# Kernel optimization log

Measured on AMD Instinct MI355X. Metric: run time of the kernel, lower is better.

## Reference

```python
import jax, jax.numpy as jnp
from jax import lax
import numpy as np

QMAX = 127.0  # int8 symmetric quant range


def setup_inputs() -> dict:
    key = jax.random.key(0)
    k1, k2, k3, k4 = jax.random.split(key, 4)
    B, S, D_in, D_out = 4, 2048, 4096, 4096
    x = jax.random.normal(k1, (B, S, D_in), dtype=jnp.float32)
    # pre-quantized per-channel weights [output_size, input_size]
    weight_q = jax.random.randint(k2, (D_out, D_in), -127, 128, dtype=jnp.int32).astype(jnp.int8)
    weight_scale = (jax.random.uniform(k3, (D_out,), dtype=jnp.float32) + 0.5) * 0.01
    bias = jax.random.normal(k4, (D_out,), dtype=jnp.float32) * 0.02
    return {"x": x, "weight_q": weight_q, "weight_scale": weight_scale, "bias": bias}


def reference(x, weight_q, weight_scale, bias):
    """Dynamic per-token int8 activation quant + int8 matmul + dequant + bias.

    x: [..., D_in] float32; weight_q: [D_out, D_in] int8;
    weight_scale: [D_out]; bias: [D_out]. Returns [..., D_out] float32.
    """
    orig_shape = x.shape
    x2 = x.reshape(-1, orig_shape[-1])  # [T, D_in]
    # dynamic per-token symmetric quantization
    amax = jnp.max(jnp.abs(x2), axis=-1, keepdims=True)  # [T, 1]
    x_scale = jnp.maximum(amax, 1e-8) / QMAX
    x_q = jnp.clip(jnp.round(x2 / x_scale), -128.0, QMAX).astype(jnp.int8)
    acc = lax.dot_general(x_q, weight_q, (((1,), (1,)), ((), ())),
                          preferred_element_type=jnp.int32)  # [T, D_out]
    out = acc.astype(jnp.float32) * x_scale * weight_scale[None, :]
    out = out.reshape(*orig_shape[:-1], out.shape[-1]) + bias
    return out
```

## Files before the change

kernel.cpp:

```cpp
#include <hip/hip_runtime.h>

typedef __attribute__((ext_vector_type(4))) int int4v;

__global__ __launch_bounds__(256) void pack_w_kernel(const int* __restrict__ w32,
                                                     int* __restrict__ w8,
                                                     long n4) {
    long i = (long)blockIdx.x * 256 + threadIdx.x;
    if (i >= n4) return;
    int4v v = ((const int4v*)w32)[i];
    w8[i] = (v[0] & 0xFF) | ((v[1] & 0xFF) << 8) |
            ((v[2] & 0xFF) << 16) | ((v[3] & 0xFF) << 24);
}

template <int NCHUNK>
__global__ __launch_bounds__(256) void quant_kernel(const float* __restrict__ x,
                                                    signed char* __restrict__ xq,
                                                    float* __restrict__ xs,
                                                    int K) {
    const int t = blockIdx.x;
    const int tid = threadIdx.x;
    const float4* row = (const float4*)(x + (size_t)t * K);

    float4 v[NCHUNK];
    float amax = 0.0f;
    #pragma unroll
    for (int i = 0; i < NCHUNK; ++i) {
        float4 f = row[i * 256 + tid];
        v[i] = f;
        amax = fmaxf(amax, fmaxf(fmaxf(fabsf(f.x), fabsf(f.y)),
                                 fmaxf(fabsf(f.z), fabsf(f.w))));
    }
    #pragma unroll
    for (int off = 32; off >= 1; off >>= 1)
        amax = fmaxf(amax, __shfl_xor(amax, off, 64));
    __shared__ float red[4];
    if ((tid & 63) == 0) red[tid >> 6] = amax;
    __syncthreads();
    amax = fmaxf(fmaxf(red[0], red[1]), fmaxf(red[2], red[3]));

    const float scale = fmaxf(amax, 1e-8f) / 127.0f;
    if (tid == 0) xs[t] = scale;
    const float inv = 1.0f / scale;

    int* orow = (int*)(xq + (size_t)t * K);
    #pragma unroll
    for (int i = 0; i < NCHUNK; ++i) {
        float4 f = v[i];
        int q0 = (int)fminf(fmaxf(rintf(f.x * inv), -128.0f), 127.0f);
        int q1 = (int)fminf(fmaxf(rintf(f.y * inv), -128.0f), 127.0f);
        int q2 = (int)fminf(fmaxf(rintf(f.z * inv), -128.0f), 127.0f);
        int q3 = (int)fminf(fmaxf(rintf(f.w * inv), -128.0f), 127.0f);
        orow[i * 256 + tid] =
            (q0 & 0xFF) | ((q1 & 0xFF) << 8) | ((q2 & 0xFF) << 16) | ((q3 & 0xFF) << 24);
    }
}

#define BM 256
#define BN 256
#define BKB 128

#define MFMA_I8 __builtin_amdgcn_mfma_i32_16x16x64_i8

#define BARRIER()                       \
    do {                                \
        __builtin_amdgcn_s_barrier();   \
        asm volatile("" ::: "memory");  \
    } while (0)

#define LGKM0() asm volatile("s_waitcnt lgkmcnt(0)" ::: "memory")
#define VMCNT4() asm volatile("s_waitcnt vmcnt(4)" ::: "memory")

#define STAGE_HALF(GL, LB, ROWOFF, KK)                                        \
    do {                                                                      \
        __builtin_amdgcn_global_load_lds(                                     \
            (const __attribute__((address_space(1))) void*)(                  \
                (GL) + (size_t)(ROWOFF) * K + (KK)),                          \
            (__attribute__((address_space(3))) void*)((LB) + (ROWOFF) * BKB), \
            16, 0, 0);                                                        \
        __builtin_amdgcn_global_load_lds(                                     \
            (const __attribute__((address_space(1))) void*)(                  \
                (GL) + (size_t)((ROWOFF) + 64) * K + (KK)),                   \
            (__attribute__((address_space(3))) void*)(                        \
                (LB) + ((ROWOFF) + 64) * BKB),                                \
            16, 0, 0);                                                        \
    } while (0)

#define LDA_KS(RP, MOFF, SW)                                               \
    do {                                                                   \
        af[0] = *(const int4v*)((RP) + ((MOFF) + 0) * 2048 + (SW));        \
        af[1] = *(const int4v*)((RP) + ((MOFF) + 1) * 2048 + (SW));        \
        af[2] = *(const int4v*)((RP) + ((MOFF) + 2) * 2048 + (SW));        \
        af[3] = *(const int4v*)((RP) + ((MOFF) + 3) * 2048 + (SW));        \
    } while (0)

#define LDB_KS(RP, KS, SW)                                                 \
    do {                                                                   \
        bf[0][(KS)] = *(const int4v*)((RP) + 0 * 2048 + (SW));             \
        bf[1][(KS)] = *(const int4v*)((RP) + 1 * 2048 + (SW));             \
        bf[2][(KS)] = *(const int4v*)((RP) + 2 * 2048 + (SW));             \
        bf[3][(KS)] = *(const int4v*)((RP) + 3 * 2048 + (SW));             \
    } while (0)

#define PH_MFMA(MB, KS)                                                       \
    do {                                                                      \
        _Pragma("unroll") for (int m_ = 0; m_ < 4; ++m_) {                    \
            _Pragma("unroll") for (int n_ = 0; n_ < 4; ++n_) {                \
                acc[(MB) + m_][n_] = MFMA_I8(af[m_], bf[n_][(KS)],            \
                                             acc[(MB) + m_][n_], 0, 0, 0);    \
            }                                                                 \
        }                                                                     \
    } while (0)

__global__ __launch_bounds__(512, 2) void gemm_i8_kernel(
    const signed char* __restrict__ A,
    const signed char* __restrict__ B,
    const float* __restrict__ xs,
    const float* __restrict__ wsc,
    const float* __restrict__ bias,
    float* __restrict__ C,
    int M, int N, int K) {
    __shared__ __align__(16) signed char lds[2][2][BM * BKB];

    const int tid = threadIdx.x;
    const int lane = tid & 63;
    const int wv = tid >> 6;
    const int wrow = wv >> 2;
    const int wcol = wv & 3;
    const int fr = lane & 15;
    const int q = lane >> 4;

    const int bm = blockIdx.y * BM;
    const int bn = blockIdx.x * BN;

    const int srow = wv * 8 + (lane >> 3);
    const int scol = ((lane & 7) ^ ((lane >> 3) & 7)) << 4;
    const signed char* gA = A + (size_t)(bm + srow) * K + scol;
    const signed char* gB = B + (size_t)(bn + srow) * K + scol;

    signed char* wA0 = &lds[0][0][0] + wv * 1024;
    signed char* wA1 = &lds[1][0][0] + wv * 1024;
    signed char* wB0 = &lds[0][1][0] + wv * 1024;
    signed char* wB1 = &lds[1][1][0] + wv * 1024;

    const int rowA = (wrow * 128 + fr) * BKB;
    const int rowB = (wcol * 64 + fr) * BKB;
    const int sw0 = ((0 + q) ^ (fr & 7)) << 4;
    const int sw1 = ((4 + q) ^ (fr & 7)) << 4;
    const signed char* rA0 = &lds[0][0][0] + rowA;
    const signed char* rA1 = &lds[1][0][0] + rowA;
    const signed char* rB0 = &lds[0][1][0] + rowB;
    const signed char* rB1 = &lds[1][1][0] + rowB;

    int4v acc[8][4];
    const int4v zero = {0, 0, 0, 0};
    #pragma unroll
    for (int m = 0; m < 8; ++m)
        #pragma unroll
        for (int n = 0; n < 4; ++n) acc[m][n] = zero;
    int4v af[4];
    int4v bf[4][2];

    STAGE_HALF(gA, wA0, 0, 0);
    STAGE_HALF(gA, wA0, 128, 0);
    STAGE_HALF(gB, wB0, 0, 0);
    STAGE_HALF(gB, wB0, 128, 0);
    STAGE_HALF(gB, wB1, 0, (size_t)BKB);
    STAGE_HALF(gB, wB1, 128, (size_t)BKB);
    VMCNT4();
    BARRIER();

    const int NT = K / BKB;
    for (int i = 0; i < NT / 2; ++i) {
        const size_t kk1 = (size_t)(2 * i + 1) * BKB;
        int t2 = 2 * i + 2; if (t2 >= NT) t2 -= NT;
        int t3 = 2 * i + 3; if (t3 >= NT) t3 -= NT;
        const size_t kk2 = (size_t)t2 * BKB;
        const size_t kk3 = (size_t)t3 * BKB;

        LDA_KS(rA0, 0, sw0);
        LDB_KS(rB0, 0, sw0);
        STAGE_HALF(gA, wA1, 0, kk1);
        BARRIER();
        LGKM0();
        __builtin_amdgcn_s_setprio(1);
        PH_MFMA(0, 0);
        __builtin_amdgcn_s_setprio(0);
        BARRIER();

        LDA_KS(rA0, 0, sw1);
        LDB_KS(rB0, 1, sw1);
        STAGE_HALF(gA, wA1, 128, kk1);
        BARRIER();
        LGKM0();
        __builtin_amdgcn_s_setprio(1);
        PH_MFMA(0, 1);
        __builtin_amdgcn_s_setprio(0);
        BARRIER();

        LDA_KS(rA0, 4, sw0);
        STAGE_HALF(gB, wB0, 0, kk2);
        BARRIER();
        LGKM0();
        __builtin_amdgcn_s_setprio(1);
        PH_MFMA(4, 0);
        __builtin_amdgcn_s_setprio(0);
        BARRIER();

        LDA_KS(rA0, 4, sw1);
        STAGE_HALF(gB, wB0, 128, kk2);
        VMCNT4();
        BARRIER();
        LGKM0();
        __builtin_amdgcn_s_setprio(1);
        PH_MFMA(4, 1);
        __builtin_amdgcn_s_setprio(0);
        BARRIER();

        LDA_KS(rA1, 0, sw0);
        LDB_KS(rB1, 0, sw0);
        STAGE_HALF(gA, wA0, 0, kk2);
        BARRIER();
        LGKM0();
        __builtin_amdgcn_s_setprio(1);
        PH_MFMA(0, 0);
        __builtin_amdgcn_s_setprio(0);
        BARRIER();

        LDA_KS(rA1, 0, sw1);
        LDB_KS(rB1, 1, sw1);
        STAGE_HALF(gA, wA0, 128, kk2);
        BARRIER();
        LGKM0();
        __builtin_amdgcn_s_setprio(1);
        PH_MFMA(0, 1);
        __builtin_amdgcn_s_setprio(0);
        BARRIER();

        LDA_KS(rA1, 4, sw0);
        STAGE_HALF(gB, wB1, 0, kk3);
        BARRIER();
        LGKM0();
        __builtin_amdgcn_s_setprio(1);
        PH_MFMA(4, 0);
        __builtin_amdgcn_s_setprio(0);
        BARRIER();

        LDA_KS(rA1, 4, sw1);
        STAGE_HALF(gB, wB1, 128, kk3);
        VMCNT4();
        BARRIER();
        LGKM0();
        __builtin_amdgcn_s_setprio(1);
        PH_MFMA(4, 1);
        __builtin_amdgcn_s_setprio(0);
        BARRIER();
    }

    asm volatile("s_waitcnt vmcnt(0)" ::: "memory");

    const int cb = bn + wcol * 64;
    float wv4[4], bv4[4];
    #pragma unroll
    for (int n = 0; n < 4; ++n) {
        wv4[n] = wsc[cb + n * 16 + fr];
        bv4[n] = bias[cb + n * 16 + fr];
    }
    #pragma unroll
    for (int m = 0; m < 8; ++m) {
        #pragma unroll
        for (int r = 0; r < 4; ++r) {
            const int row = bm + wrow * 128 + m * 16 + q * 4 + r;
            const float s = xs[row];
            float* crow = C + (size_t)row * N + cb + fr;
            #pragma unroll
            for (int n = 0; n < 4; ++n)
                crow[n * 16] = (float)acc[m][n][r] * s * wv4[n] + bv4[n];
        }
    }
}

extern "C" void kernel_launch(void* const* d_in, const int* in_sizes, int n_in,
                              void* d_out, int out_size, void* d_ws, size_t ws_size,
                              hipStream_t stream) {
    const float* x = (const float*)d_in[0];
    const int* wq32 = (const int*)d_in[1];
    const float* wscale = (const float*)d_in[2];
    const float* bias = (const float*)d_in[3];
    float* out = (float*)d_out;

    const int d_out_dim = in_sizes[2];
    const int d_in_dim = in_sizes[1] / d_out_dim;
    const int T = in_sizes[0] / d_in_dim;

    const size_t wbytes = (size_t)d_out_dim * d_in_dim;
    signed char* w8 = (signed char*)d_ws;
    signed char* xq = (signed char*)d_ws + wbytes;
    float* xscl = (float*)((char*)d_ws + wbytes + (size_t)T * d_in_dim);

    const long n4 = (long)d_out_dim * d_in_dim / 4;
    pack_w_kernel<<<(int)((n4 + 255) / 256), 256, 0, stream>>>(wq32, (int*)w8, n4);

    if (d_in_dim == 4096) {
        quant_kernel<4><<<T, 256, 0, stream>>>(x, xq, xscl, d_in_dim);
    } else {
        quant_kernel<8><<<T, 256, 0, stream>>>(x, xq, xscl, d_in_dim);
    }

    dim3 grid(d_out_dim / BN, T / BM);
    gemm_i8_kernel<<<grid, 512, 0, stream>>>(xq, w8, xscl, wscale, bias, out,
                                             T, d_out_dim, d_in_dim);
}
```

Before: 379.8 us.

## Double-buffer MFMA A/B fragments to overlap LDS reads with MFMA phases

Adds register double-buffering for the A fragments (af[2][4]) so each phase's LDS reads for the next MFMA group are issued before the current group's MFMAs run. The explicit lgkmcnt(0) waits are removed, leaving the compiler to insert the needed waits. LDS reads for the next buffer's first phase are moved after the vmcnt wait and barrier so the new global loads are visible. This uses more VGPRs, which risks spills under launch_bounds(512,2). It also depends on the compiler placing correct lgkm waits relative to the barriers.

```diff
diff --git a/kernel.cpp b/kernel.cpp
--- a/kernel.cpp
+++ b/kernel.cpp
@@ -67,7 +67,6 @@
         asm volatile("" ::: "memory");  \
     } while (0)
 
-#define LGKM0() asm volatile("s_waitcnt lgkmcnt(0)" ::: "memory")
 #define VMCNT4() asm volatile("s_waitcnt vmcnt(4)" ::: "memory")
 
 #define STAGE_HALF(GL, LB, ROWOFF, KK)                                        \
@@ -85,15 +84,15 @@
             16, 0, 0);                                                        \
     } while (0)
 
-#define LDA_KS(RP, MOFF, SW)                                               \
+#define LDA_KS(AF, RP, MOFF, SW)                                           \
     do {                                                                   \
-        af[0] = *(const int4v*)((RP) + ((MOFF) + 0) * 2048 + (SW));        \
-        af[1] = *(const int4v*)((RP) + ((MOFF) + 1) * 2048 + (SW));        \
-        af[2] = *(const int4v*)((RP) + ((MOFF) + 2) * 2048 + (SW));        \
-        af[3] = *(const int4v*)((RP) + ((MOFF) + 3) * 2048 + (SW));        \
-    } while (0)
-
-#define LDB_KS(RP, KS, SW)                                                 \
+        AF[0] = *(const int4v*)((RP) + ((MOFF) + 0) * 2048 + (SW));        \
+        AF[1] = *(const int4v*)((RP) + ((MOFF) + 1) * 2048 + (SW));        \
+        AF[2] = *(const int4v*)((RP) + ((MOFF) + 2) * 2048 + (SW));        \
+        AF[3] = *(const int4v*)((RP) + ((MOFF) + 3) * 2048 + (SW));        \
+    } while (0)
+
+#define LDB_KS(KS, RP, SW)                                                 \
     do {                                                                   \
         bf[0][(KS)] = *(const int4v*)((RP) + 0 * 2048 + (SW));             \
         bf[1][(KS)] = *(const int4v*)((RP) + 1 * 2048 + (SW));             \
@@ -101,11 +100,11 @@
         bf[3][(KS)] = *(const int4v*)((RP) + 3 * 2048 + (SW));             \
     } while (0)
 
-#define PH_MFMA(MB, KS)                                                       \
+#define PH_MFMA(MB, KS, AF)                                                   \
     do {                                                                      \
         _Pragma("unroll") for (int m_ = 0; m_ < 4; ++m_) {                    \
             _Pragma("unroll") for (int n_ = 0; n_ < 4; ++n_) {                \
-                acc[(MB) + m_][n_] = MFMA_I8(af[m_], bf[n_][(KS)],            \
+                acc[(MB) + m_][n_] = MFMA_I8(AF[m_], bf[n_][(KS)],            \
                                              acc[(MB) + m_][n_], 0, 0, 0);    \
             }                                                                 \
         }                                                                     \
@@ -157,7 +156,7 @@
     for (int m = 0; m < 8; ++m)
         #pragma unroll
         for (int n = 0; n < 4; ++n) acc[m][n] = zero;
-    int4v af[4];
+    int4v af[2][4];
     int4v bf[4][2];
 
     STAGE_HALF(gA, wA0, 0, 0);
@@ -169,6 +168,9 @@
     VMCNT4();
     BARRIER();
 
+    LDA_KS(af[0], rA0, 0, sw0);
+    LDB_KS(0, rB0, sw0);
+
     const int NT = K / BKB;
     for (int i = 0; i < NT / 2; ++i) {
         const size_t kk1 = (size_t)(2 * i + 1) * BKB;
@@ -177,81 +179,73 @@
         const size_t kk2 = (size_t)t2 * BKB;
         const size_t kk3 = (size_t)t3 * BKB;
 
-        LDA_KS(rA0, 0, sw0);
-        LDB_KS(rB0, 0, sw0);
+        LDA_KS(af[1], rA0, 0, sw1);
+        LDB_KS(1, rB0, sw1);
         STAGE_HALF(gA, wA1, 0, kk1);
         BARRIER();
-        LGKM0();
-        __builtin_amdgcn_s_setprio(1);
-        PH_MFMA(0, 0);
-        __builtin_amdgcn_s_setprio(0);
-        BARRIER();
-
-        LDA_KS(rA0, 0, sw1);
-        LDB_KS(rB0, 1, sw1);
+        __builtin_amdgcn_s_setprio(1);
+        PH_MFMA(0, 0, af[0]);
+        __builtin_amdgcn_s_setprio(0);
+        BARRIER();
+
+        LDA_KS(af[0], rA0, 4, sw0);
         STAGE_HALF(gA, wA1, 128, kk1);
         BARRIER();
-        LGKM0();
-        __builtin_amdgcn_s_setprio(1);
-        PH_MFMA(0, 1);
-        __builtin_amdgcn_s_setprio(0);
-        BARRIER();
-
-        LDA_KS(rA0, 4, sw0);
+        __builtin_amdgcn_s_setprio(1);
+        PH_MFMA(0, 1, af[1]);
+        __builtin_amdgcn_s_setprio(0);
+        BARRIER();
+
+        LDA_KS(af[1], rA0, 4, sw1);
         STAGE_HALF(gB, wB0, 0, kk2);
         BARRIER();
-        LGKM0();
-        __builtin_amdgcn_s_setprio(1);
-        PH_MFMA(4, 0);
-        __builtin_amdgcn_s_setprio(0);
-        BARRIER();
-
-        LDA_KS(rA0, 4, sw1);
+        __builtin_amdgcn_s_setprio(1);
+        PH_MFMA(4, 0, af[0]);
+        __builtin_amdgcn_s_setprio(0);
+        BARRIER();
+
         STAGE_HALF(gB, wB0, 128, kk2);
         VMCNT4();
         BARRIER();
-        LGKM0();
-        __builtin_amdgcn_s_setprio(1);
-        PH_MFMA(4, 1);
-        __builtin_amdgcn_s_setprio(0);
-        BARRIER();
-
-        LDA_KS(rA1, 0, sw0);
-        LDB_KS(rB1, 0, sw0);
+        LDA_KS(af[0], rA1, 0, sw0);
+        LDB_KS(0, rB1, sw0);
+        __builtin_amdgcn_s_setprio(1);
+        PH_MFMA(4, 1, af[1]);
+        __builtin_amdgcn_s_setprio(0);
+        BARRIER();
+
+        LDA_KS(af[1], rA1, 0, sw1);
+        LDB_KS(1, rB1, sw1);
         STAGE_HALF(gA, wA0, 0, kk2);
         BARRIER();
-        LGKM0();
-        __builtin_amdgcn_s_setprio(1);
-        PH_MFMA(0, 0);
-        __builtin_amdgcn_s_setprio(0);
-        BARRIER();
-
-        LDA_KS(rA1, 0, sw1);
-        LDB_KS(rB1, 1, sw1);
+        __builtin_amdgcn_s_setprio(1);
+        PH_MFMA(0, 0, af[0]);
+        __builtin_amdgcn_s_setprio(0);
+        BARRIER();
+
+        LDA_KS(af[0], rA1, 4, sw0);
         STAGE_HALF(gA, wA0, 128, kk2);
         BARRIER();
-        LGKM0();
-        __builtin_amdgcn_s_setprio(1);
-        PH_MFMA(0, 1);
-        __builtin_amdgcn_s_setprio(0);
-        BARRIER();
-
-        LDA_KS(rA1, 4, sw0);
+        __builtin_amdgcn_s_setprio(1);
+        PH_MFMA(0, 1, af[1]);
+        __builtin_amdgcn_s_setprio(0);
+        BARRIER();
+
+        LDA_KS(af[1], rA1, 4, sw1);
         STAGE_HALF(gB, wB1, 0, kk3);
         BARRIER();
-        LGKM0();
-        __builtin_amdgcn_s_setprio(1);
-        PH_MFMA(4, 0);
-        __builtin_amdgcn_s_setprio(0);
-        BARRIER();
-
-        LDA_KS(rA1, 4, sw1);
+        __builtin_amdgcn_s_setprio(1);
+        PH_MFMA(4, 0, af[0]);
+        __builtin_amdgcn_s_setprio(0);
+        BARRIER();
+
         STAGE_HALF(gB, wB1, 128, kk3);
         VMCNT4();
         BARRIER();
-        LGKM0();
-        __builtin_amdgcn_s_setprio(1);
-        PH_MFMA(4, 1);
+        LDA_KS(af[0], rA0, 0, sw0);
+        LDB_KS(0, rB0, sw0);
+        __builtin_amdgcn_s_setprio(1);
+        PH_MFMA(4, 1, af[1]);
         __builtin_amdgcn_s_setprio(0);
         BARRIER();
     }
```

Measured after the change: 375.0 us. About the same (-1.2%).
